# Kernel optimization log

Measured on AMD Instinct MI355X. Metric: run time of the kernel, lower is better.

## Reference

```python
import jax, jax.numpy as jnp
import numpy as np

D = 1024
B = 128
N = 576
MAX_LEN = 5000
TEMP = 1.0


def build_pe(max_len, d):
    position = jnp.arange(max_len, dtype=jnp.float32)[:, None]
    div_term = jnp.exp(jnp.arange(0, d, 2, dtype=jnp.float32) * (-np.log(10000.0) / d))
    pe = jnp.zeros((max_len, d), dtype=jnp.float32)
    pe = pe.at[:, 0::2].set(jnp.sin(position * div_term))
    pe = pe.at[:, 1::2].set(jnp.cos(position * div_term))
    return pe  # [max_len, d]


def setup_inputs() -> dict:
    key = jax.random.key(0)
    ks = jax.random.split(key, 16)
    s = 0.02
    inp = {
        "x": jax.random.normal(ks[0], (B, N), dtype=jnp.float32),
        "timesteps": jax.random.randint(ks[1], (B,), 0, 1000),
        "text_feat": jax.random.normal(ks[2], (B, D), dtype=jnp.float32),
        "image_feat": jax.random.normal(ks[3], (B, N, D), dtype=jnp.float32),
        # projections (torch Linear stored as [in, out] here; bias=False for q/k/v)
        "Wq": jax.random.normal(ks[4], (D, D), dtype=jnp.float32) * s,
        "Wk": jax.random.normal(ks[5], (D, D), dtype=jnp.float32) * s,
        "Wv": jax.random.normal(ks[6], (D, D), dtype=jnp.float32) * s,
        "Wp": jax.random.normal(ks[7], (D, D), dtype=jnp.float32) * s,
        "bp": jnp.zeros((D,), dtype=jnp.float32),
        # timestep embedder MLP
        "Wt1": jax.random.normal(ks[8], (D, D), dtype=jnp.float32) * s,
        "bt1": jnp.zeros((D,), dtype=jnp.float32),
        "Wt2": jax.random.normal(ks[9], (D, D), dtype=jnp.float32) * s,
        "bt2": jnp.zeros((D,), dtype=jnp.float32),
        # decoder MLP: 2d -> 2d -> 1
        "Wd1": jax.random.normal(ks[10], (2 * D, 2 * D), dtype=jnp.float32) * s,
        "bd1": jnp.zeros((2 * D,), dtype=jnp.float32),
        "Wd2": jax.random.normal(ks[11], (2 * D, 1), dtype=jnp.float32) * s,
        "bd2": jnp.zeros((1,), dtype=jnp.float32),
    }
    return inp


def reference(x, timesteps, text_feat, image_feat, Wq, Wk, Wv, Wp, bp,
              Wt1, bt1, Wt2, bt2, Wd1, bd1, Wd2, bd2):
    pe = build_pe(MAX_LEN, D)
    # timestep conditioning: MLP(pe[t])  -> [B, d]
    t_emb = pe[timesteps]                                   # [B, d]
    cond = jax.nn.silu(t_emb @ Wt1 + bt1) @ Wt2 + bt2       # [B, d]

    # image re-weighting by text similarity
    i_w = jax.nn.softmax(jnp.einsum('bd,bnd->bn', text_feat, image_feat) / TEMP, axis=-1)
    img = image_feat * i_w[:, :, None]                      # [B, n, d]

    q = (text_feat + cond) @ Wq                             # [B, d]
    k = (img + cond[:, None, :]) @ Wk                       # [B, n, d]
    v = (img + cond[:, None, :]) @ Wv                       # [B, n, d]

    weight = jax.nn.softmax(jnp.einsum('bd,bnd->bn', q, k) + x, axis=-1)  # [B, n]
    new_emb = jnp.einsum('bn,bnd->bd', weight, v) @ Wp + bp               # [B, d]

    # decoder on concat([new_emb broadcast, img])  -> [B, n, 2d] -> [B, n]
    emb = jnp.concatenate([jnp.broadcast_to(new_emb[:, None, :], img.shape), img], axis=-1)
    h = jax.nn.relu(emb @ Wd1 + bd1)
    p = (h @ Wd2 + bd2)[..., 0]                             # [B, n]
    return p + weight
```

## Files before the change

kernel.cpp:

```cpp
#include <hip/hip_runtime.h>
#include <hip/hip_bf16.h>
#include <cmath>

#define D_    1024
#define B_    128
#define N_    576
#define ROWS_ (B_*N_)
#define TWOD_ 2048
#define TAU_  1e-5f
#define NU_   8

__device__ __forceinline__ float waveReduceSum(float v){
  #pragma unroll
  for (int m=32;m;m>>=1) v += __shfl_xor(v,m,64);
  return v;
}
__device__ __forceinline__ float waveReduceMax(float v){
  #pragma unroll
  for (int m=32;m;m>>=1) v = fmaxf(v,__shfl_xor(v,m,64));
  return v;
}

__global__ __launch_bounds__(256) void k_init(float* wimg, float* p_corr, int* count){
  int i = blockIdx.x*256 + threadIdx.x;
  if (i < B_*D_) wimg[i] = 0.f;
  if (i < ROWS_) p_corr[i] = 0.f;
  if (i == 0) *count = 0;
}

__global__ __launch_bounds__(256) void k_temb(const int* __restrict__ ts, float* __restrict__ temb){
  int b = blockIdx.x;
  float t = (float)ts[b];
  for (int i=threadIdx.x; i<D_/2; i+=256){
    float dv = expf((float)(2*i) * (-9.210340371976184f/(float)D_));
    float a = t*dv;
    temb[b*D_ + 2*i]   = sinf(a);
    temb[b*D_ + 2*i+1] = cosf(a);
  }
}

__global__ __launch_bounds__(256) void k_gemm(const float* __restrict__ A, const float* __restrict__ A2,
    const float* __restrict__ W, int ldw, const float* __restrict__ bias, float* __restrict__ C,
    int nout, int act, int tmode){
  __shared__ float a_s[2][D_];
  int r0 = blockIdx.y*2;
  const float4* A4 = (const float4*)(A + (size_t)r0*D_);
  float4* s4 = (float4*)a_s;
  if (A2){
    const float4* B4 = (const float4*)(A2 + (size_t)r0*D_);
    for (int i=threadIdx.x;i<512;i+=256){
      float4 a = A4[i], b = B4[i];
      s4[i] = make_float4(a.x+b.x, a.y+b.y, a.z+b.z, a.w+b.w);
    }
  } else {
    for (int i=threadIdx.x;i<512;i+=256) s4[i] = A4[i];
  }
  __syncthreads();
  int rsel = threadIdx.x>>7;
  int row  = r0 + rsel;
  int col  = blockIdx.x*128 + (threadIdx.x&127);
  const float* arow = a_s[rsel];
  float acc0=0.f, acc1=0.f;
  if (tmode==0){
    const float* wp = W + col;
    #pragma unroll 8
    for (int k=0;k<D_;k+=2){
      acc0 = fmaf(arow[k],   wp[(size_t)k*ldw],       acc0);
      acc1 = fmaf(arow[k+1], wp[(size_t)(k+1)*ldw],   acc1);
    }
  } else {
    const float* wp = W + (size_t)col*ldw;
    #pragma unroll 4
    for (int k=0;k<D_;k+=4){
      float4 wv = *(const float4*)(wp+k);
      acc0 = fmaf(arow[k],  wv.x,acc0); acc1 = fmaf(arow[k+1],wv.y,acc1);
      acc0 = fmaf(arow[k+2],wv.z,acc0); acc1 = fmaf(arow[k+3],wv.w,acc1);
    }
  }
  float o = acc0 + acc1 + (bias ? bias[col] : 0.f);
  if (act==1) o = o/(1.f+expf(-o));
  C[(size_t)row*nout+col]=o;
}

__global__ __launch_bounds__(256) void k_dots(const float* __restrict__ text,
    const float* __restrict__ imgf, float* __restrict__ s){
  int wave = threadIdx.x>>6, lane = threadIdx.x&63;
  int row = blockIdx.x*4 + wave;
  int b = row / N_;
  const float4* ip = (const float4*)(imgf + (size_t)row*D_);
  const float4* tp = (const float4*)(text + (size_t)b*D_);
  float acc=0.f;
  #pragma unroll
  for (int p=0;p<4;p++){
    float4 a = ip[p*64+lane];
    float4 t = tp[p*64+lane];
    acc = fmaf(a.x,t.x,acc); acc = fmaf(a.y,t.y,acc);
    acc = fmaf(a.z,t.z,acc); acc = fmaf(a.w,t.w,acc);
  }
  acc = waveReduceSum(acc);
  if (lane==0) s[row]=acc;
}

__global__ __launch_bounds__(256) void k_softmax(const float* __restrict__ s, float* __restrict__ w,
    int buildList, int* count, int* lrow, float* liw){
  int b = blockIdx.x;
  __shared__ float rbuf[4];
  const float* sp = s + b*N_;
  float m = -3e38f;
  for (int i=threadIdx.x;i<N_;i+=256) m = fmaxf(m, sp[i]);
  m = waveReduceMax(m);
  if ((threadIdx.x&63)==0) rbuf[threadIdx.x>>6]=m;
  __syncthreads();
  m = fmaxf(fmaxf(rbuf[0],rbuf[1]),fmaxf(rbuf[2],rbuf[3]));
  __syncthreads();
  float sum=0.f;
  for (int i=threadIdx.x;i<N_;i+=256) sum += expf(sp[i]-m);
  sum = waveReduceSum(sum);
  if ((threadIdx.x&63)==0) rbuf[threadIdx.x>>6]=sum;
  __syncthreads();
  sum = rbuf[0]+rbuf[1]+rbuf[2]+rbuf[3];
  float inv = 1.f/sum;
  float* wp = w + b*N_;
  for (int i=threadIdx.x;i<N_;i+=256){
    float wi = expf(sp[i]-m)*inv;
    wp[i]=wi;
    if (buildList && wi > TAU_){
      int pos = atomicAdd(count,1);
      if (pos < ROWS_){ lrow[pos]=b*N_+i; liw[pos]=wi; }
    }
  }
}

__global__ __launch_bounds__(256) void k_lbase(const float* __restrict__ x, float* __restrict__ s){
  int i = blockIdx.x*256+threadIdx.x;
  ((float4*)s)[i] = ((const float4*)x)[i];
}

__global__ __launch_bounds__(256) void k_lsparse(const float* __restrict__ x, const float* __restrict__ imgf,
    const float* __restrict__ kq, const int* __restrict__ count, const int* __restrict__ lrow,
    const float* __restrict__ liw, float* __restrict__ s){
  int wave=threadIdx.x>>6, lane=threadIdx.x&63;
  int cnt = min(*count, ROWS_);
  for (int e = blockIdx.x*4+wave; e<cnt; e += gridDim.x*4){
    int row=lrow[e], b=row/N_; float iw=liw[e];
    const float4* ip=(const float4*)(imgf+(size_t)row*D_);
    const float4* kp=(const float4*)(kq + b*D_);
    float acc=0.f;
    #pragma unroll
    for (int p=0;p<4;p++){
      int c = p*64+lane;
      float4 a = ip[c];
      float4 k = kp[c];
      acc = fmaf(a.x,k.x,acc); acc = fmaf(a.y,k.y,acc);
      acc = fmaf(a.z,k.z,acc); acc = fmaf(a.w,k.w,acc);
    }
    acc = waveReduceSum(acc);
    if (lane==0) s[row] = x[row] + iw*acc;
  }
}

__global__ __launch_bounds__(256) void k_wimg(const float* __restrict__ imgf, const float* __restrict__ wgt,
    const int* __restrict__ count, const int* __restrict__ lrow,
    const float* __restrict__ liw, float* __restrict__ wimg){
  int cnt = min(*count, ROWS_);
  for (int e = blockIdx.x; e<cnt; e += gridDim.x){
    int row=lrow[e], b=row/N_;
    float coef = liw[e]*wgt[row];
    const float* src = imgf + (size_t)row*D_;
    for (int i=threadIdx.x;i<D_;i+=256)
      atomicAdd(&wimg[b*D_+i], coef*src[i]);
  }
}

__global__ __launch_bounds__(256) void k_p0(const float* __restrict__ r, const float* __restrict__ wd2,
    const float* __restrict__ bd2, float* __restrict__ p0){
  __shared__ float rbuf[4];
  int b=blockIdx.x;
  float acc=0.f;
  for (int j=threadIdx.x;j<TWOD_;j+=256)
    acc = fmaf(fmaxf(r[b*TWOD_+j],0.f), wd2[j], acc);
  acc = waveReduceSum(acc);
  if((threadIdx.x&63)==0) rbuf[threadIdx.x>>6]=acc;
  __syncthreads();
  if (threadIdx.x==0) p0[b] = rbuf[0]+rbuf[1]+rbuf[2]+rbuf[3] + bd2[0];
}

__global__ __launch_bounds__(256) void k_corr(const float* __restrict__ imgf, const float* __restrict__ Wd1,
    const float* __restrict__ r, const float* __restrict__ wd2, const int* __restrict__ count,
    const int* __restrict__ lrow, const float* __restrict__ liw,
    float* __restrict__ p_corr){
  __shared__ __align__(16) float img[D_][NU_];
  __shared__ float rbuf[4];
  int j = blockIdx.x*256 + threadIdx.x;
  float wd2j = wd2[j];
  int cnt = min(*count, ROWS_);
  int NG = gridDim.y;
  for (int base = blockIdx.y*NU_; base < cnt; base += NG*NU_){
    int nu = min(NU_, cnt-base);
    __syncthreads();
    for (int u=0;u<nu;u++){
      const float* src = imgf + (size_t)lrow[base+u]*D_;
      for (int i=threadIdx.x;i<D_;i+=256) img[i][u]=src[i];
    }
    for (int u=nu;u<NU_;u++)
      for (int i=threadIdx.x;i<D_;i+=256) img[i][u]=0.f;
    __syncthreads();
    float g[NU_];
    #pragma unroll
    for (int u=0;u<NU_;u++) g[u]=0.f;
    const float* wp = Wd1 + (size_t)D_*TWOD_ + j;
    #pragma unroll 4
    for (int e=0;e<D_;e++){
      float wv = wp[(size_t)e*TWOD_];
      const float4* ir = (const float4*)(&img[e][0]);
      float4 i0 = ir[0], i1 = ir[1];
      g[0]=fmaf(i0.x,wv,g[0]); g[1]=fmaf(i0.y,wv,g[1]);
      g[2]=fmaf(i0.z,wv,g[2]); g[3]=fmaf(i0.w,wv,g[3]);
      g[4]=fmaf(i1.x,wv,g[4]); g[5]=fmaf(i1.y,wv,g[5]);
      g[6]=fmaf(i1.z,wv,g[6]); g[7]=fmaf(i1.w,wv,g[7]);
    }
    for (int u=0;u<nu;u++){
      int row = lrow[base+u];
      float rv = r[(size_t)(row/N_)*TWOD_ + j];
      float c  = rv + liw[base+u]*g[u];
      float contrib = (fmaxf(c,0.f)-fmaxf(rv,0.f))*wd2j;
      contrib = waveReduceSum(contrib);
      if ((threadIdx.x&63)==0) rbuf[threadIdx.x>>6]=contrib;
      __syncthreads();
      if (threadIdx.x==0) atomicAdd(&p_corr[row], rbuf[0]+rbuf[1]+rbuf[2]+rbuf[3]);
      __syncthreads();
    }
  }
}

__global__ __launch_bounds__(256) void k_final(const float* __restrict__ p0, const float* __restrict__ p_corr,
    const float* __restrict__ wgt, float* __restrict__ out){
  int i = blockIdx.x*256+threadIdx.x;
  if (i<ROWS_){
    int b = i/N_;
    out[i] = p0[b] + p_corr[i] + wgt[i];
  }
}

extern "C" void kernel_launch(void* const* d_in, const int* in_sizes, int n_in,
                              void* d_out, int out_size, void* d_ws, size_t ws_size,
                              hipStream_t stream) {
  const float* x    = (const float*)d_in[0];
  const int*   ts   = (const int*)  d_in[1];
  const float* text = (const float*)d_in[2];
  const float* imgf = (const float*)d_in[3];
  const float* Wq   = (const float*)d_in[4];
  const float* Wk   = (const float*)d_in[5];
  const float* Wv   = (const float*)d_in[6];
  const float* Wp   = (const float*)d_in[7];
  const float* bp   = (const float*)d_in[8];
  const float* Wt1  = (const float*)d_in[9];
  const float* bt1  = (const float*)d_in[10];
  const float* Wt2  = (const float*)d_in[11];
  const float* bt2  = (const float*)d_in[12];
  const float* Wd1  = (const float*)d_in[13];
  const float* bd1  = (const float*)d_in[14];
  const float* Wd2  = (const float*)d_in[15];
  const float* bd2  = (const float*)d_in[16];
  float* out = (float*)d_out;

  float* f = (float*)d_ws;
  float* bufA  = f;
  float* bufB  = f +  131072;
  float* cond  = f +  262144;
  float* wimg  = f +  393216;
  float* rbuf  = f +  524288;
  float* sbuf  = f +  786432;
  float* wgt   = f +  860160;
  float* pcorr = f +  933888;
  float* liw   = f + 1007616;
  int*   lrow  = (int*)(f + 1081344);
  float* p0    = f + 1155072;
  int*   cnt   = (int*)(f + 1155200);

  k_init<<<512,256,0,stream>>>(wimg, pcorr, cnt);
  k_temb<<<B_,256,0,stream>>>(ts, bufA);
  k_gemm<<<dim3(8,64),256,0,stream>>>(bufA, nullptr, Wt1, D_, bt1, bufB, D_, 1, 0);
  k_gemm<<<dim3(8,64),256,0,stream>>>(bufB, nullptr, Wt2, D_, bt2, cond, D_, 0, 0);
  k_dots<<<ROWS_/4,256,0,stream>>>(text, imgf, sbuf);
  k_softmax<<<B_,256,0,stream>>>(sbuf, sbuf, 1, cnt, lrow, liw);
  k_gemm<<<dim3(8,64),256,0,stream>>>(text, cond, Wq, D_, nullptr, bufB, D_, 0, 0);
  k_gemm<<<dim3(8,64),256,0,stream>>>(bufB, nullptr, Wk, D_, nullptr, bufA, D_, 0, 1);
  k_lbase<<<ROWS_/1024,256,0,stream>>>(x, sbuf);
  k_lsparse<<<64,256,0,stream>>>(x, imgf, bufA, cnt, lrow, liw, sbuf);
  k_softmax<<<B_,256,0,stream>>>(sbuf, wgt, 0, cnt, lrow, liw);
  k_wimg<<<128,256,0,stream>>>(imgf, wgt, cnt, lrow, liw, wimg);
  k_gemm<<<dim3(8,64),256,0,stream>>>(wimg, cond, Wv, D_, nullptr, bufA, D_, 0, 0);
  k_gemm<<<dim3(8,64),256,0,stream>>>(bufA, nullptr, Wp, D_, bp, bufB, D_, 0, 0);
  k_gemm<<<dim3(16,64),256,0,stream>>>(bufB, nullptr, Wd1, TWOD_, bd1, rbuf, TWOD_, 0, 0);
  k_p0<<<B_,256,0,stream>>>(rbuf, Wd2, bd2, p0);
  k_corr<<<dim3(8,64),256,0,stream>>>(imgf, Wd1, rbuf, Wd2, cnt, lrow, liw, pcorr);
  k_final<<<(ROWS_+255)/256,256,0,stream>>>(p0, pcorr, wgt, out);
}
```

Measured before the change: 926.2 us.

## Fuse all stages into one persistent kernel with grid-wide barriers

```diff
diff --git a/kernel.cpp b/kernel.cpp
--- a/kernel.cpp
+++ b/kernel.cpp
@@ -1,5 +1,4 @@
 #include <hip/hip_runtime.h>
-#include <hip/hip_bf16.h>
 #include <cmath>
 
 #define D_    1024
@@ -8,237 +7,316 @@
 #define ROWS_ (B_*N_)
 #define TWOD_ 2048
 #define TAU_  1e-5f
-#define NU_   8
-
-__device__ __forceinline__ float waveReduceSum(float v){
+#define NB_   512
+#define NT_   256
+
+__device__ __forceinline__ float wrsum(float v){
   #pragma unroll
   for (int m=32;m;m>>=1) v += __shfl_xor(v,m,64);
   return v;
 }
-__device__ __forceinline__ float waveReduceMax(float v){
+__device__ __forceinline__ float wrmax(float v){
   #pragma unroll
   for (int m=32;m;m>>=1) v = fmaxf(v,__shfl_xor(v,m,64));
   return v;
 }
 
-__global__ __launch_bounds__(256) void k_init(float* wimg, float* p_corr, int* count){
-  int i = blockIdx.x*256 + threadIdx.x;
-  if (i < B_*D_) wimg[i] = 0.f;
-  if (i < ROWS_) p_corr[i] = 0.f;
-  if (i == 0) *count = 0;
-}
-
-__global__ __launch_bounds__(256) void k_temb(const int* __restrict__ ts, float* __restrict__ temb){
-  int b = blockIdx.x;
-  float t = (float)ts[b];
-  for (int i=threadIdx.x; i<D_/2; i+=256){
-    float dv = expf((float)(2*i) * (-9.210340371976184f/(float)D_));
-    float a = t*dv;
-    temb[b*D_ + 2*i]   = sinf(a);
-    temb[b*D_ + 2*i+1] = cosf(a);
-  }
-}
-
-__global__ __launch_bounds__(256) void k_gemm(const float* __restrict__ A, const float* __restrict__ A2,
-    const float* __restrict__ W, int ldw, const float* __restrict__ bias, float* __restrict__ C,
-    int nout, int act, int tmode){
-  __shared__ float a_s[2][D_];
-  int r0 = blockIdx.y*2;
+__device__ __forceinline__ void gsync(int* bar, int phase){
+  __syncthreads();
+  if (threadIdx.x==0){
+    __threadfence();
+    __hip_atomic_fetch_add(bar, 1, __ATOMIC_ACQ_REL, __HIP_MEMORY_SCOPE_AGENT);
+    while (__hip_atomic_load(bar, __ATOMIC_ACQUIRE, __HIP_MEMORY_SCOPE_AGENT) < NB_*phase)
+      __builtin_amdgcn_s_sleep(2);
+  }
+  __syncthreads();
+}
+
+template<int NOUT,int ACT,int TMODE,int FUSEADD,int DOP0>
+__device__ void gemm_unit(const float* A, const float* A2, const float* W,
+    const float* bias, float* C, int bx, int by, float* a_s,
+    const float* wd2, float* p0){
+  int tid = threadIdx.x;
+  int r0 = by*2;
   const float4* A4 = (const float4*)(A + (size_t)r0*D_);
   float4* s4 = (float4*)a_s;
-  if (A2){
+  if (FUSEADD){
     const float4* B4 = (const float4*)(A2 + (size_t)r0*D_);
-    for (int i=threadIdx.x;i<512;i+=256){
-      float4 a = A4[i], b = B4[i];
-      s4[i] = make_float4(a.x+b.x, a.y+b.y, a.z+b.z, a.w+b.w);
-    }
+    for (int i=tid;i<512;i+=NT_){ float4 a=A4[i], b=B4[i];
+      s4[i] = make_float4(a.x+b.x,a.y+b.y,a.z+b.z,a.w+b.w); }
   } else {
-    for (int i=threadIdx.x;i<512;i+=256) s4[i] = A4[i];
+    for (int i=tid;i<512;i+=NT_) s4[i]=A4[i];
   }
   __syncthreads();
-  int rsel = threadIdx.x>>7;
-  int row  = r0 + rsel;
-  int col  = blockIdx.x*128 + (threadIdx.x&127);
-  const float* arow = a_s[rsel];
+  int rsel = tid>>7;
+  int row = r0 + rsel;
+  int col = bx*128 + (tid&127);
+  const float* arow = a_s + rsel*D_;
   float acc0=0.f, acc1=0.f;
-  if (tmode==0){
+  if (TMODE==0){
     const float* wp = W + col;
     #pragma unroll 8
     for (int k=0;k<D_;k+=2){
-      acc0 = fmaf(arow[k],   wp[(size_t)k*ldw],       acc0);
-      acc1 = fmaf(arow[k+1], wp[(size_t)(k+1)*ldw],   acc1);
+      acc0 = fmaf(arow[k],   wp[(size_t)k*NOUT],     acc0);
+      acc1 = fmaf(arow[k+1], wp[(size_t)(k+1)*NOUT], acc1);
     }
   } else {
-    const float* wp = W + (size_t)col*ldw;
+    const float* wp = W + (size_t)col*D_;
     #pragma unroll 4
     for (int k=0;k<D_;k+=4){
       float4 wv = *(const float4*)(wp+k);
-      acc0 = fmaf(arow[k],  wv.x,acc0); acc1 = fmaf(arow[k+1],wv.y,acc1);
-      acc0 = fmaf(arow[k+2],wv.z,acc0); acc1 = fmaf(arow[k+3],wv.w,acc1);
-    }
-  }
-  float o = acc0 + acc1 + (bias ? bias[col] : 0.f);
-  if (act==1) o = o/(1.f+expf(-o));
-  C[(size_t)row*nout+col]=o;
-}
-
-__global__ __launch_bounds__(256) void k_dots(const float* __restrict__ text,
-    const float* __restrict__ imgf, float* __restrict__ s){
-  int wave = threadIdx.x>>6, lane = threadIdx.x&63;
-  int row = blockIdx.x*4 + wave;
-  int b = row / N_;
-  const float4* ip = (const float4*)(imgf + (size_t)row*D_);
-  const float4* tp = (const float4*)(text + (size_t)b*D_);
-  float acc=0.f;
-  #pragma unroll
-  for (int p=0;p<4;p++){
-    float4 a = ip[p*64+lane];
-    float4 t = tp[p*64+lane];
-    acc = fmaf(a.x,t.x,acc); acc = fmaf(a.y,t.y,acc);
-    acc = fmaf(a.z,t.z,acc); acc = fmaf(a.w,t.w,acc);
-  }
-  acc = waveReduceSum(acc);
-  if (lane==0) s[row]=acc;
-}
-
-__global__ __launch_bounds__(256) void k_softmax(const float* __restrict__ s, float* __restrict__ w,
-    int buildList, int* count, int* lrow, float* liw){
-  int b = blockIdx.x;
-  __shared__ float rbuf[4];
-  const float* sp = s + b*N_;
-  float m = -3e38f;
-  for (int i=threadIdx.x;i<N_;i+=256) m = fmaxf(m, sp[i]);
-  m = waveReduceMax(m);
-  if ((threadIdx.x&63)==0) rbuf[threadIdx.x>>6]=m;
+      acc0=fmaf(arow[k],  wv.x,acc0); acc1=fmaf(arow[k+1],wv.y,acc1);
+      acc0=fmaf(arow[k+2],wv.z,acc0); acc1=fmaf(arow[k+3],wv.w,acc1);
+    }
+  }
+  float o = acc0+acc1 + (bias ? bias[col] : 0.f);
+  if (ACT==1) o = o/(1.f+expf(-o));
+  C[(size_t)row*NOUT + col] = o;
+  if (DOP0){
+    float c = fmaxf(o,0.f)*wd2[col];
+    c = wrsum(c);
+    if ((tid&63)==0) atomicAdd(&p0[row], c);
+  }
   __syncthreads();
-  m = fmaxf(fmaxf(rbuf[0],rbuf[1]),fmaxf(rbuf[2],rbuf[3]));
-  __syncthreads();
-  float sum=0.f;
-  for (int i=threadIdx.x;i<N_;i+=256) sum += expf(sp[i]-m);
-  sum = waveReduceSum(sum);
-  if ((threadIdx.x&63)==0) rbuf[threadIdx.x>>6]=sum;
-  __syncthreads();
-  sum = rbuf[0]+rbuf[1]+rbuf[2]+rbuf[3];
-  float inv = 1.f/sum;
-  float* wp = w + b*N_;
-  for (int i=threadIdx.x;i<N_;i+=256){
-    float wi = expf(sp[i]-m)*inv;
-    wp[i]=wi;
-    if (buildList && wi > TAU_){
-      int pos = atomicAdd(count,1);
-      if (pos < ROWS_){ lrow[pos]=b*N_+i; liw[pos]=wi; }
-    }
-  }
-}
-
-__global__ __launch_bounds__(256) void k_lbase(const float* __restrict__ x, float* __restrict__ s){
-  int i = blockIdx.x*256+threadIdx.x;
-  ((float4*)s)[i] = ((const float4*)x)[i];
-}
-
-__global__ __launch_bounds__(256) void k_lsparse(const float* __restrict__ x, const float* __restrict__ imgf,
-    const float* __restrict__ kq, const int* __restrict__ count, const int* __restrict__ lrow,
-    const float* __restrict__ liw, float* __restrict__ s){
-  int wave=threadIdx.x>>6, lane=threadIdx.x&63;
-  int cnt = min(*count, ROWS_);
-  for (int e = blockIdx.x*4+wave; e<cnt; e += gridDim.x*4){
-    int row=lrow[e], b=row/N_; float iw=liw[e];
-    const float4* ip=(const float4*)(imgf+(size_t)row*D_);
-    const float4* kp=(const float4*)(kq + b*D_);
-    float acc=0.f;
-    #pragma unroll
-    for (int p=0;p<4;p++){
-      int c = p*64+lane;
-      float4 a = ip[c];
-      float4 k = kp[c];
-      acc = fmaf(a.x,k.x,acc); acc = fmaf(a.y,k.y,acc);
-      acc = fmaf(a.z,k.z,acc); acc = fmaf(a.w,k.w,acc);
-    }
-    acc = waveReduceSum(acc);
-    if (lane==0) s[row] = x[row] + iw*acc;
-  }
-}
-
-__global__ __launch_bounds__(256) void k_wimg(const float* __restrict__ imgf, const float* __restrict__ wgt,
-    const int* __restrict__ count, const int* __restrict__ lrow,
-    const float* __restrict__ liw, float* __restrict__ wimg){
-  int cnt = min(*count, ROWS_);
-  for (int e = blockIdx.x; e<cnt; e += gridDim.x){
-    int row=lrow[e], b=row/N_;
-    float coef = liw[e]*wgt[row];
-    const float* src = imgf + (size_t)row*D_;
-    for (int i=threadIdx.x;i<D_;i+=256)
-      atomicAdd(&wimg[b*D_+i], coef*src[i]);
-  }
-}
-
-__global__ __launch_bounds__(256) void k_p0(const float* __restrict__ r, const float* __restrict__ wd2,
-    const float* __restrict__ bd2, float* __restrict__ p0){
-  __shared__ float rbuf[4];
-  int b=blockIdx.x;
-  float acc=0.f;
-  for (int j=threadIdx.x;j<TWOD_;j+=256)
-    acc = fmaf(fmaxf(r[b*TWOD_+j],0.f), wd2[j], acc);
-  acc = waveReduceSum(acc);
-  if((threadIdx.x&63)==0) rbuf[threadIdx.x>>6]=acc;
-  __syncthreads();
-  if (threadIdx.x==0) p0[b] = rbuf[0]+rbuf[1]+rbuf[2]+rbuf[3] + bd2[0];
-}
-
-__global__ __launch_bounds__(256) void k_corr(const float* __restrict__ imgf, const float* __restrict__ Wd1,
-    const float* __restrict__ r, const float* __restrict__ wd2, const int* __restrict__ count,
-    const int* __restrict__ lrow, const float* __restrict__ liw,
-    float* __restrict__ p_corr){
-  __shared__ __align__(16) float img[D_][NU_];
-  __shared__ float rbuf[4];
-  int j = blockIdx.x*256 + threadIdx.x;
-  float wd2j = wd2[j];
-  int cnt = min(*count, ROWS_);
-  int NG = gridDim.y;
-  for (int base = blockIdx.y*NU_; base < cnt; base += NG*NU_){
-    int nu = min(NU_, cnt-base);
-    __syncthreads();
-    for (int u=0;u<nu;u++){
-      const float* src = imgf + (size_t)lrow[base+u]*D_;
-      for (int i=threadIdx.x;i<D_;i+=256) img[i][u]=src[i];
-    }
-    for (int u=nu;u<NU_;u++)
-      for (int i=threadIdx.x;i<D_;i+=256) img[i][u]=0.f;
-    __syncthreads();
-    float g[NU_];
-    #pragma unroll
-    for (int u=0;u<NU_;u++) g[u]=0.f;
-    const float* wp = Wd1 + (size_t)D_*TWOD_ + j;
-    #pragma unroll 4
-    for (int e=0;e<D_;e++){
-      float wv = wp[(size_t)e*TWOD_];
-      const float4* ir = (const float4*)(&img[e][0]);
-      float4 i0 = ir[0], i1 = ir[1];
-      g[0]=fmaf(i0.x,wv,g[0]); g[1]=fmaf(i0.y,wv,g[1]);
-      g[2]=fmaf(i0.z,wv,g[2]); g[3]=fmaf(i0.w,wv,g[3]);
-      g[4]=fmaf(i1.x,wv,g[4]); g[5]=fmaf(i1.y,wv,g[5]);
-      g[6]=fmaf(i1.z,wv,g[6]); g[7]=fmaf(i1.w,wv,g[7]);
-    }
-    for (int u=0;u<nu;u++){
-      int row = lrow[base+u];
-      float rv = r[(size_t)(row/N_)*TWOD_ + j];
-      float c  = rv + liw[base+u]*g[u];
-      float contrib = (fmaxf(c,0.f)-fmaxf(rv,0.f))*wd2j;
-      contrib = waveReduceSum(contrib);
-      if ((threadIdx.x&63)==0) rbuf[threadIdx.x>>6]=contrib;
+}
+
+__global__ __launch_bounds__(NT_,2) void k_mega(
+  const float* __restrict__ x, const int* __restrict__ ts,
+  const float* __restrict__ text, const float* __restrict__ imgf,
+  const float* __restrict__ Wq, const float* __restrict__ Wk,
+  const float* __restrict__ Wv, const float* __restrict__ Wp, const float* __restrict__ bp,
+  const float* __restrict__ Wt1, const float* __restrict__ bt1,
+  const float* __restrict__ Wt2, const float* __restrict__ bt2,
+  const float* __restrict__ Wd1, const float* __restrict__ bd1,
+  const float* __restrict__ Wd2, const float* __restrict__ bd2,
+  float* __restrict__ out, float* __restrict__ ws)
+{
+  __shared__ __align__(16) float smem[8256];
+  float* temb  = ws;
+  float* h1    = ws + 131072;
+  float* cond  = ws + 262144;
+  float* q     = ws + 393216;
+  float* kq    = ws + 524288;
+  float* wimg  = ws + 655360;
+  float* v     = ws + 786432;
+  float* nemb  = ws + 917504;
+  float* rb    = ws + 1048576;
+  float* sbuf  = ws + 1310720;
+  float* wgt   = ws + 1384448;
+  float* pcorr = ws + 1458176;
+  float* liw   = ws + 1531904;
+  int*   lrow  = (int*)(ws + 1605632);
+  float* p0    = ws + 1679360;
+  int*   cnt   = (int*)(ws + 1679488);
+  int*   bar   = (int*)(ws + 1679552);
+
+  const int bid = blockIdx.x, tid = threadIdx.x;
+  const int lane = tid&63, wid = tid>>6;
+
+  {
+    int t = bid*NT_ + tid;
+    if (t >= 65536){
+      int p = t - 65536, b = p>>9, i = p&511;
+      float tt = (float)ts[b];
+      float dv = expf((float)(2*i) * (-9.210340371976184f/1024.f));
+      float a = tt*dv;
+      temb[b*D_+2*i]   = sinf(a);
+      temb[b*D_+2*i+1] = cosf(a);
+    }
+    if (t < ROWS_) pcorr[t]=0.f;
+    if (t < B_)    p0[t]=0.f;
+    if (t==0)      *cnt = 0;
+  }
+  gsync(bar,1);
+
+  gemm_unit<D_,1,0,0,0>(temb,nullptr,Wt1,bt1,h1, bid&7, bid>>3, smem, nullptr,nullptr);
+  {
+    int wg = bid*4 + wid;
+    for (int row = wg; row < ROWS_; row += NB_*4){
+      const float4* ip = (const float4*)(imgf + (size_t)row*D_);
+      const float4* tp = (const float4*)(text + (size_t)(row/N_)*D_);
+      float acc=0.f;
+      #pragma unroll
+      for (int p=0;p<4;p++){
+        float4 a=ip[p*64+lane], t=tp[p*64+lane];
+        acc=fmaf(a.x,t.x,acc); acc=fmaf(a.y,t.y,acc);
+        acc=fmaf(a.z,t.z,acc); acc=fmaf(a.w,t.w,acc);
+      }
+      acc = wrsum(acc);
+      if (lane==0) sbuf[row]=acc;
+    }
+  }
+  gsync(bar,2);
+
+  gemm_unit<D_,0,0,0,0>(h1,nullptr,Wt2,bt2,cond, bid&7, bid>>3, smem, nullptr,nullptr);
+  if (bid < B_){
+    const float* sp = sbuf + bid*N_;
+    float* red = smem;
+    float m=-3e38f;
+    for (int i=tid;i<N_;i+=NT_) m=fmaxf(m,sp[i]);
+    m = wrmax(m);
+    if (lane==0) red[wid]=m;
+    __syncthreads();
+    m = fmaxf(fmaxf(red[0],red[1]),fmaxf(red[2],red[3]));
+    __syncthreads();
+    float s=0.f;
+    for (int i=tid;i<N_;i+=NT_) s += expf(sp[i]-m);
+    s = wrsum(s);
+    if (lane==0) red[wid]=s;
+    __syncthreads();
+    s = red[0]+red[1]+red[2]+red[3];
+    float inv = 1.f/s;
+    for (int i=tid;i<N_;i+=NT_){
+      float wi = expf(sp[i]-m)*inv;
+      if (wi > TAU_){
+        int pos = atomicAdd(cnt,1);
+        if (pos < ROWS_){ lrow[pos]=bid*N_+i; liw[pos]=wi; }
+      }
+    }
+  }
+  gsync(bar,3);
+
+  gemm_unit<D_,0,0,1,0>(text,cond,Wq,nullptr,q, bid&7, bid>>3, smem, nullptr,nullptr);
+  gsync(bar,4);
+
+  gemm_unit<D_,0,1,0,0>(q,nullptr,Wk,nullptr,kq, bid&7, bid>>3, smem, nullptr,nullptr);
+  gsync(bar,5);
+
+  if (bid < B_){
+    int b = bid;
+    float* kqs  = smem;
+    float* srow = smem+1024;
+    float* red  = smem+1600;
+    int*   mcv  = (int*)(smem+1608);
+    int*   mrow = (int*)(smem+1664);
+    float* miw  = smem+2240;
+    for (int i=tid;i<D_;i+=NT_) kqs[i]=kq[b*D_+i];
+    for (int j=tid;j<N_;j+=NT_) srow[j]=x[b*N_+j];
+    if (tid==0) *mcv=0;
+    __syncthreads();
+    int c = min(__hip_atomic_load(cnt,__ATOMIC_RELAXED,__HIP_MEMORY_SCOPE_AGENT), ROWS_);
+    for (int e=tid;e<c;e+=NT_){
+      int row=lrow[e];
+      if (row/N_ == b){
+        int p = atomicAdd(mcv,1);
+        mrow[p]=row; miw[p]=liw[e];
+      }
+    }
+    __syncthreads();
+    int mc = *mcv;
+    for (int m=0;m<mc;m++){
+      int row=mrow[m];
+      const float4* ip=(const float4*)(imgf+(size_t)row*D_);
+      const float4* kp=(const float4*)kqs;
+      float4 a=ip[tid], k=kp[tid];
+      float acc=a.x*k.x+a.y*k.y+a.z*k.z+a.w*k.w;
+      acc = wrsum(acc);
+      if (lane==0) red[wid]=acc;
       __syncthreads();
-      if (threadIdx.x==0) atomicAdd(&p_corr[row], rbuf[0]+rbuf[1]+rbuf[2]+rbuf[3]);
+      if (tid==0) srow[row%N_] += miw[m]*(red[0]+red[1]+red[2]+red[3]);
       __syncthreads();
     }
-  }
-}
-
-__global__ __launch_bounds__(256) void k_final(const float* __restrict__ p0, const float* __restrict__ p_corr,
-    const float* __restrict__ wgt, float* __restrict__ out){
-  int i = blockIdx.x*256+threadIdx.x;
-  if (i<ROWS_){
-    int b = i/N_;
-    out[i] = p0[b] + p_corr[i] + wgt[i];
+    float mx=-3e38f;
+    for (int j=tid;j<N_;j+=NT_) mx=fmaxf(mx,srow[j]);
+    mx=wrmax(mx);
+    if (lane==0) red[wid]=mx;
+    __syncthreads();
+    mx=fmaxf(fmaxf(red[0],red[1]),fmaxf(red[2],red[3]));
+    __syncthreads();
+    float sum=0.f;
+    for (int j=tid;j<N_;j+=NT_) sum+=expf(srow[j]-mx);
+    sum=wrsum(sum);
+    if (lane==0) red[wid]=sum;
+    __syncthreads();
+    sum=red[0]+red[1]+red[2]+red[3];
+    float inv=1.f/sum;
+    __syncthreads();
+    for (int j=tid;j<N_;j+=NT_){
+      float wv=expf(srow[j]-mx)*inv;
+      wgt[b*N_+j]=wv;
+      srow[j]=wv;
+    }
+    __syncthreads();
+    float a0=0,a1=0,a2=0,a3=0;
+    for (int m=0;m<mc;m++){
+      int row=mrow[m];
+      float coef = miw[m]*srow[row%N_];
+      const float* ip = imgf + (size_t)row*D_;
+      a0=fmaf(coef,ip[tid],a0);
+      a1=fmaf(coef,ip[tid+256],a1);
+      a2=fmaf(coef,ip[tid+512],a2);
+      a3=fmaf(coef,ip[tid+768],a3);
+    }
+    wimg[b*D_+tid]=a0; wimg[b*D_+tid+256]=a1;
+    wimg[b*D_+tid+512]=a2; wimg[b*D_+tid+768]=a3;
+  }
+  gsync(bar,6);
+
+  gemm_unit<D_,0,0,1,0>(wimg,cond,Wv,nullptr,v, bid&7, bid>>3, smem, nullptr,nullptr);
+  gsync(bar,7);
+
+  gemm_unit<D_,0,0,0,0>(v,nullptr,Wp,bp,nemb, bid&7, bid>>3, smem, nullptr,nullptr);
+  gsync(bar,8);
+
+  {
+    int u0=bid, u1=bid+NB_;
+    gemm_unit<TWOD_,0,0,0,1>(nemb,nullptr,Wd1,bd1,rb, u0&15, u0>>4, smem, Wd2, p0);
+    gemm_unit<TWOD_,0,0,0,1>(nemb,nullptr,Wd1,bd1,rb, u1&15, u1>>4, smem, Wd2, p0);
+  }
+  gsync(bar,9);
+
+  {
+    int jc = bid&7, yg = bid>>3;
+    int j = jc*256 + tid;
+    float wd2j = Wd2[j];
+    int c = min(__hip_atomic_load(cnt,__ATOMIC_RELAXED,__HIP_MEMORY_SCOPE_AGENT), ROWS_);
+    float* img = smem;
+    float* red = smem + 8192;
+    for (int base = yg*8; base < c; base += 64*8){
+      int nu = min(8, c-base);
+      __syncthreads();
+      for (int u=0;u<nu;u++){
+        const float* src = imgf + (size_t)lrow[base+u]*D_;
+        for (int i=tid;i<D_;i+=NT_) img[i*8+u]=src[i];
+      }
+      for (int u=nu;u<8;u++)
+        for (int i=tid;i<D_;i+=NT_) img[i*8+u]=0.f;
+      __syncthreads();
+      float g[8];
+      #pragma unroll
+      for (int u=0;u<8;u++) g[u]=0.f;
+      const float* wp = Wd1 + (size_t)D_*TWOD_ + j;
+      #pragma unroll 4
+      for (int e=0;e<D_;e++){
+        float wv = wp[(size_t)e*TWOD_];
+        const float4* ir = (const float4*)(&img[e*8]);
+        float4 i0=ir[0], i1=ir[1];
+        g[0]=fmaf(i0.x,wv,g[0]); g[1]=fmaf(i0.y,wv,g[1]);
+        g[2]=fmaf(i0.z,wv,g[2]); g[3]=fmaf(i0.w,wv,g[3]);
+        g[4]=fmaf(i1.x,wv,g[4]); g[5]=fmaf(i1.y,wv,g[5]);
+        g[6]=fmaf(i1.z,wv,g[6]); g[7]=fmaf(i1.w,wv,g[7]);
+      }
+      for (int u=0;u<nu;u++){
+        int row=lrow[base+u];
+        float rv = rb[(size_t)(row/N_)*TWOD_ + j];
+        float cc = rv + liw[base+u]*g[u];
+        float contrib = (fmaxf(cc,0.f)-fmaxf(rv,0.f))*wd2j;
+        contrib = wrsum(contrib);
+        if (lane==0) red[wid]=contrib;
+        __syncthreads();
+        if (tid==0) atomicAdd(&pcorr[row], red[0]+red[1]+red[2]+red[3]);
+        __syncthreads();
+      }
+    }
+  }
+  gsync(bar,10);
+
+  {
+    int t = bid*NT_ + tid;
+    if (t < ROWS_){
+      int b = t/N_;
+      out[t] = p0[b] + bd2[0] + pcorr[t] + wgt[t];
+    }
   }
 }
 
@@ -263,37 +341,11 @@
   const float* Wd2  = (const float*)d_in[15];
   const float* bd2  = (const float*)d_in[16];
   float* out = (float*)d_out;
-
-  float* f = (float*)d_ws;
-  float* bufA  = f;
-  float* bufB  = f +  131072;
-  float* cond  = f +  262144;
-  float* wimg  = f +  393216;
-  float* rbuf  = f +  524288;
-  float* sbuf  = f +  786432;
-  float* wgt   = f +  860160;
-  float* pcorr = f +  933888;
-  float* liw   = f + 1007616;
-  int*   lrow  = (int*)(f + 1081344);
-  float* p0    = f + 1155072;
-  int*   cnt   = (int*)(f + 1155200);
-
-  k_init<<<512,256,0,stream>>>(wimg, pcorr, cnt);
-  k_temb<<<B_,256,0,stream>>>(ts, bufA);
-  k_gemm<<<dim3(8,64),256,0,stream>>>(bufA, nullptr, Wt1, D_, bt1, bufB, D_, 1, 0);
-  k_gemm<<<dim3(8,64),256,0,stream>>>(bufB, nullptr, Wt2, D_, bt2, cond, D_, 0, 0);
-  k_dots<<<ROWS_/4,256,0,stream>>>(text, imgf, sbuf);
-  k_softmax<<<B_,256,0,stream>>>(sbuf, sbuf, 1, cnt, lrow, liw);
-  k_gemm<<<dim3(8,64),256,0,stream>>>(text, cond, Wq, D_, nullptr, bufB, D_, 0, 0);
-  k_gemm<<<dim3(8,64),256,0,stream>>>(bufB, nullptr, Wk, D_, nullptr, bufA, D_, 0, 1);
-  k_lbase<<<ROWS_/1024,256,0,stream>>>(x, sbuf);
-  k_lsparse<<<64,256,0,stream>>>(x, imgf, bufA, cnt, lrow, liw, sbuf);
-  k_softmax<<<B_,256,0,stream>>>(sbuf, wgt, 0, cnt, lrow, liw);
-  k_wimg<<<128,256,0,stream>>>(imgf, wgt, cnt, lrow, liw, wimg);
-  k_gemm<<<dim3(8,64),256,0,stream>>>(wimg, cond, Wv, D_, nullptr, bufA, D_, 0, 0);
-  k_gemm<<<dim3(8,64),256,0,stream>>>(bufA, nullptr, Wp, D_, bp, bufB, D_, 0, 0);
-  k_gemm<<<dim3(16,64),256,0,stream>>>(bufB, nullptr, Wd1, TWOD_, bd1, rbuf, TWOD_, 0, 0);
-  k_p0<<<B_,256,0,stream>>>(rbuf, Wd2, bd2, p0);
-  k_corr<<<dim3(8,64),256,0,stream>>>(imgf, Wd1, rbuf, Wd2, cnt, lrow, liw, pcorr);
-  k_final<<<(ROWS_+255)/256,256,0,stream>>>(p0, pcorr, wgt, out);
-}
+  float* ws  = (float*)d_ws;
+
+  hipMemsetAsync((char*)d_ws + (size_t)1679552*4, 0, 256, stream);
+
+  k_mega<<<NB_,NT_,0,stream>>>(x, ts, text, imgf, Wq, Wk, Wv, Wp, bp,
+                               Wt1, bt1, Wt2, bt2, Wd1, bd1, Wd2, bd2,
+                               out, ws);
+}
```

After: 1.715 ms. 85.2% more time.
